# Optimization experiments

Hardware: AMD Instinct MI355X
Metric: run time of the kernel (lower is better)

Reference implementation:

```python
import jax, jax.numpy as jnp
import numpy as np

VOCAB = 28996
EMBED = 512
N = 8192


def setup_inputs() -> dict:
    key = jax.random.key(0)
    k1, k2, k3, k4 = jax.random.split(key, 4)
    x = jax.random.normal(k1, (N, EMBED), dtype=jnp.float32)
    y = jax.random.randint(k2, (N,), 0, VOCAB, dtype=jnp.int64 if jax.config.jax_enable_x64 else jnp.int32)
    # nn.Linear params: weight (vocab, embed), bias (vocab,)
    W = jax.random.normal(k3, (VOCAB, EMBED), dtype=jnp.float32) * 0.02
    b = jax.random.normal(k4, (VOCAB,), dtype=jnp.float32) * 0.02
    return {"x": x, "y": y, "W": W, "b": b}


def reference(x, y, W, b):
    # Decoder: linear -> softmax over vocab (dim=1)
    logits = jnp.einsum("ne,ve->nv", x, W) + b          # (N, VOCAB)
    probs = jax.nn.softmax(logits, axis=1)              # first softmax (faithful to original)
    # nn.CrossEntropyLoss applied to probs: mean over nodes of
    #   logsumexp(probs) - probs[y]   (i.e., -log_softmax(probs)[y])
    logp = jax.nn.log_softmax(probs, axis=1)            # second (redundant) softmax pass
    nll = -jnp.take_along_axis(logp, y[:, None].astype(jnp.int32), axis=1)[:, 0]
    return jnp.mean(nll)
```

## Files before the change

### kernel.cpp

```cpp
#include <hip/hip_runtime.h>
#include <stdint.h>

#define VOCAB 28996
#define EMBED 512
#define NROWS 8192
#define VPAD  29056
#define LOG2E 1.4426950408889634f
#define WSCALE 16.0f
#define INV_WSCALE_L2E (LOG2E / 16.0f)

typedef __attribute__((ext_vector_type(4)))  int   i32x4;
typedef __attribute__((ext_vector_type(8)))  int   i32x8;
typedef __attribute__((ext_vector_type(16))) float f32x16;

__device__ __forceinline__ void gload_lds16(const void* g, void* l) {
  __builtin_amdgcn_global_load_lds(
      (__attribute__((address_space(1))) const void*)g,
      (__attribute__((address_space(3))) void*)l, 16, 0, 0);
}

__device__ __forceinline__ int pk_fp8x4(float a, float b, float c, float d) {
  int r = __builtin_amdgcn_cvt_pk_fp8_f32(a, b, 0, false);
  r = __builtin_amdgcn_cvt_pk_fp8_f32(c, d, r, true);
  return r;
}

__global__ void __launch_bounds__(256)
prep_kernel(const float* __restrict__ x, const float* __restrict__ W,
            const float* __restrict__ b, const int* __restrict__ y,
            int* __restrict__ xb, int* __restrict__ wb,
            float* __restrict__ py, float* __restrict__ sg) {
  const int bid = blockIdx.x;
  if (bid < 7264) {
    int i = (bid * 256 + threadIdx.x) * 8;
    const int VK = VOCAB * EMBED;
    int2 o;
    if (i < VK) {
      float4 v0 = *(const float4*)(W + i);
      float4 v1 = *(const float4*)(W + i + 4);
      o.x = pk_fp8x4(v0.x * WSCALE, v0.y * WSCALE, v0.z * WSCALE, v0.w * WSCALE);
      o.y = pk_fp8x4(v1.x * WSCALE, v1.y * WSCALE, v1.z * WSCALE, v1.w * WSCALE);
    } else { o.x = 0; o.y = 0; }
    *(int2*)(wb + i / 4) = o;
  } else if (bid < 9312) {
    int i = ((bid - 7264) * 256 + threadIdx.x) * 8;
    float4 v0 = *(const float4*)(x + i);
    float4 v1 = *(const float4*)(x + i + 4);
    int2 o;
    o.x = pk_fp8x4(v0.x, v0.y, v0.z, v0.w);
    o.y = pk_fp8x4(v1.x, v1.y, v1.z, v1.w);
    *(int2*)(xb + i / 4) = o;
  } else if (bid < 11360) {
    const int row  = ((bid - 9312) * 256 + threadIdx.x) >> 6;
    const int lane = threadIdx.x & 63;
    const int yr = y[row];
    const float4* xr = (const float4*)(x + (size_t)row * EMBED);
    const float4* wr = (const float4*)(W + (size_t)yr * EMBED);
    float d = 0.f;
#pragma unroll
    for (int t = 0; t < 2; ++t) {
      float4 a = xr[lane * 2 + t], c = wr[lane * 2 + t];
      d += a.x * c.x + a.y * c.y + a.z * c.z + a.w * c.w;
    }
#pragma unroll
    for (int m = 1; m < 64; m <<= 1) d += __shfl_xor(d, m);
    if (lane == 0) py[row] = __expf(d + b[yr]);
  } else {
    int i = (bid - 11360) * 256 + threadIdx.x;
    sg[i] = 0.f;
  }
}

__global__ void __launch_bounds__(256, 4)
gemm_stats_kernel(const uint8_t* __restrict__ xb, const uint8_t* __restrict__ wb,
                  const float* __restrict__ bias, float* __restrict__ sg) {
  __shared__ uint8_t lA[128 * 128];
  __shared__ uint8_t lB[128 * 128];

  const int tid  = threadIdx.x;
  const int lane = tid & 63;
  const int w    = tid >> 6;
  const int l31  = lane & 31;
  const int h    = lane >> 5;
  const int kx   = lane & 7;
  const int wr   = (w >> 1) * 64;
  const int wc   = (w & 1) * 64;
  const int rowBase = blockIdx.x * 128;
  const int colBase = blockIdx.y * 128;

  f32x16 acc[2][2];
#pragma unroll
  for (int i = 0; i < 2; ++i)
#pragma unroll
    for (int j = 0; j < 2; ++j)
#pragma unroll
      for (int r = 0; r < 16; ++r) acc[i][j][r] = 0.f;

  const int srow = lane >> 3;
  const int skel = ((lane & 7) ^ srow) * 16;

  const int aBase = (wr + l31) * 128;
  const int bBase = (wc + l31) * 128;

  for (int kt = 0; kt < 4; ++kt) {
    const int k0 = kt * 128;
#pragma unroll
    for (int t = 0; t < 4; ++t) {
      const int c = w * 4 + t;
      const int r = c * 8 + srow;
      gload_lds16(xb + (size_t)(rowBase + r) * EMBED + k0 + skel, &lA[c * 1024]);
      gload_lds16(wb + (size_t)(colBase + r) * EMBED + k0 + skel, &lB[c * 1024]);
    }
    __syncthreads();
#pragma unroll
    for (int kk = 0; kk < 2; ++kk) {
      const int c0 = ((kk * 4 + h * 2) ^ kx) << 4;
      const int c1 = c0 ^ 16;
      i32x8 bq[2];
#pragma unroll
      for (int jj = 0; jj < 2; ++jj) {
        const int base = bBase + jj * 32 * 128;
        i32x4 lo = *(const i32x4*)&lB[base + c0];
        i32x4 hi = *(const i32x4*)&lB[base + c1];
        bq[jj] = __builtin_shufflevector(lo, hi, 0, 1, 2, 3, 4, 5, 6, 7);
      }
#pragma unroll
      for (int ii = 0; ii < 2; ++ii) {
        const int base = aBase + ii * 32 * 128;
        i32x4 lo = *(const i32x4*)&lA[base + c0];
        i32x4 hi = *(const i32x4*)&lA[base + c1];
        i32x8 af = __builtin_shufflevector(lo, hi, 0, 1, 2, 3, 4, 5, 6, 7);
        acc[ii][0] = __builtin_amdgcn_mfma_scale_f32_32x32x64_f8f6f4(
            af, bq[0], acc[ii][0], 0, 0, 0, 0x7F7F7F7F, 0, 0x7F7F7F7F);
        acc[ii][1] = __builtin_amdgcn_mfma_scale_f32_32x32x64_f8f6f4(
            af, bq[1], acc[ii][1], 0, 0, 0, 0x7F7F7F7F, 0, 0x7F7F7F7F);
      }
    }
    __syncthreads();
  }

  float bvl[2];
#pragma unroll
  for (int jj = 0; jj < 2; ++jj) {
    const int col = colBase + wc + jj * 32 + l31;
    bvl[jj] = (col < VOCAB) ? bias[col] * LOG2E : -1e30f;
  }

  float sp[32];
#pragma unroll
  for (int ii = 0; ii < 2; ++ii)
#pragma unroll
    for (int r = 0; r < 16; ++r)
      sp[ii * 16 + r] = exp2f(fmaf(acc[ii][0][r], INV_WSCALE_L2E, bvl[0])) +
                        exp2f(fmaf(acc[ii][1][r], INV_WSCALE_L2E, bvl[1]));

  float t1[16];
#pragma unroll
  for (int u = 0; u < 16; ++u) {
    float a = sp[2 * u]     + __shfl_xor(sp[2 * u],     1);
    float b = sp[2 * u + 1] + __shfl_xor(sp[2 * u + 1], 1);
    t1[u] = (l31 & 1) ? b : a;
  }
  float t2[8];
#pragma unroll
  for (int u = 0; u < 8; ++u) {
    float a = t1[2 * u]     + __shfl_xor(t1[2 * u],     2);
    float b = t1[2 * u + 1] + __shfl_xor(t1[2 * u + 1], 2);
    t2[u] = (l31 & 2) ? b : a;
  }
  float t3[4];
#pragma unroll
  for (int u = 0; u < 4; ++u) {
    float a = t2[2 * u]     + __shfl_xor(t2[2 * u],     4);
    float b = t2[2 * u + 1] + __shfl_xor(t2[2 * u + 1], 4);
    t3[u] = (l31 & 4) ? b : a;
  }
  float t4[2];
#pragma unroll
  for (int u = 0; u < 2; ++u) {
    float a = t3[2 * u]     + __shfl_xor(t3[2 * u],     8);
    float b = t3[2 * u + 1] + __shfl_xor(t3[2 * u + 1], 8);
    t4[u] = (l31 & 8) ? b : a;
  }
  {
    float a = t4[0] + __shfl_xor(t4[0], 16);
    float b = t4[1] + __shfl_xor(t4[1], 16);
    float ssum = (l31 & 16) ? b : a;
    const int v = l31;
    const int row = rowBase + wr + (v >> 4) * 32 + (v & 3) + 8 * ((v & 15) >> 2) + 4 * h;
    atomicAdd(&sg[row], ssum);
  }
}

__global__ void finalize_kernel(const float* __restrict__ sg, const float* __restrict__ py,
                                float* __restrict__ out) {
  __shared__ float red[256];
  float a = 0.f;
  for (int i = threadIdx.x; i < NROWS; i += 256)
    a += py[i] / sg[i];
  red[threadIdx.x] = a;
  __syncthreads();
  for (int st = 128; st > 0; st >>= 1) {
    if (threadIdx.x < st) red[threadIdx.x] += red[threadIdx.x + st];
    __syncthreads();
  }
  if (threadIdx.x == 0)
    out[0] = logf((float)(VOCAB + 1)) - red[0] * (1.f / (float)NROWS);
}

extern "C" void kernel_launch(void* const* d_in, const int* in_sizes, int n_in,
                              void* d_out, int out_size, void* d_ws, size_t ws_size,
                              hipStream_t stream) {
  const float* x = (const float*)d_in[0];
  const int*   y = (const int*)d_in[1];
  const float* W = (const float*)d_in[2];
  const float* b = (const float*)d_in[3];

  char* ws = (char*)d_ws;
  uint8_t* xb = (uint8_t*)ws;
  uint8_t* wb = (uint8_t*)(ws + 4194304);
  float*   sg = (float*)(ws + 4194304 + 14876672);
  float*   py = sg + NROWS;

  prep_kernel<<<11392, 256, 0, stream>>>(x, W, b, y, (int*)xb, (int*)wb, py, sg);
  gemm_stats_kernel<<<dim3(64, 227), 256, 0, stream>>>(xb, wb, b, sg);
  finalize_kernel<<<1, 256, 0, stream>>>(sg, py, (float*)d_out);
}
```

Baseline: 269.6 us.

## Fuse finalize into GEMM via last-block atomic counter; batch LDS fragment loads

Removes the separate single-block finalize launch. Each GEMM block now increments a global counter after its atomic row-sum updates, and the last block to finish computes the final loss reduction. The counter is reset in the prep kernel. Inner-loop LDS reads are also reordered so all A/B fragment halves are loaded before the MFMAs issue. The gain is one fewer kernel launch, paid for with an extra agent-scope atomic in every block.

```diff
diff --git a/kernel.cpp b/kernel.cpp
--- a/kernel.cpp
+++ b/kernel.cpp
@@ -8,6 +8,7 @@
 #define LOG2E 1.4426950408889634f
 #define WSCALE 16.0f
 #define INV_WSCALE_L2E (LOG2E / 16.0f)
+#define GEMM_BLOCKS (64 * 227)
 
 typedef __attribute__((ext_vector_type(4)))  int   i32x4;
 typedef __attribute__((ext_vector_type(8)))  int   i32x8;
@@ -29,7 +30,8 @@
 prep_kernel(const float* __restrict__ x, const float* __restrict__ W,
             const float* __restrict__ b, const int* __restrict__ y,
             int* __restrict__ xb, int* __restrict__ wb,
-            float* __restrict__ py, float* __restrict__ sg) {
+            float* __restrict__ py, float* __restrict__ sg,
+            unsigned* __restrict__ counter) {
   const int bid = blockIdx.x;
   if (bid < 7264) {
     int i = (bid * 256 + threadIdx.x) * 8;
@@ -68,14 +70,18 @@
   } else {
     int i = (bid - 11360) * 256 + threadIdx.x;
     sg[i] = 0.f;
+    if (bid == 11360 && threadIdx.x == 0) *counter = 0u;
   }
 }
 
 __global__ void __launch_bounds__(256, 4)
 gemm_stats_kernel(const uint8_t* __restrict__ xb, const uint8_t* __restrict__ wb,
-                  const float* __restrict__ bias, float* __restrict__ sg) {
+                  const float* __restrict__ bias, float* __restrict__ sg,
+                  const float* __restrict__ py, unsigned* __restrict__ counter,
+                  float* __restrict__ out) {
   __shared__ uint8_t lA[128 * 128];
   __shared__ uint8_t lB[128 * 128];
+  __shared__ bool amLast;
 
   const int tid  = threadIdx.x;
   const int lane = tid & 63;
@@ -116,24 +122,24 @@
     for (int kk = 0; kk < 2; ++kk) {
       const int c0 = ((kk * 4 + h * 2) ^ kx) << 4;
       const int c1 = c0 ^ 16;
-      i32x8 bq[2];
-#pragma unroll
-      for (int jj = 0; jj < 2; ++jj) {
-        const int base = bBase + jj * 32 * 128;
-        i32x4 lo = *(const i32x4*)&lB[base + c0];
-        i32x4 hi = *(const i32x4*)&lB[base + c1];
-        bq[jj] = __builtin_shufflevector(lo, hi, 0, 1, 2, 3, 4, 5, 6, 7);
-      }
+      i32x4 blo[2], bhi[2], alo[2], ahi[2];
+#pragma unroll
+      for (int jj = 0; jj < 2; ++jj) blo[jj] = *(const i32x4*)&lB[bBase + jj * 4096 + c0];
+#pragma unroll
+      for (int ii = 0; ii < 2; ++ii) alo[ii] = *(const i32x4*)&lA[aBase + ii * 4096 + c0];
+#pragma unroll
+      for (int jj = 0; jj < 2; ++jj) bhi[jj] = *(const i32x4*)&lB[bBase + jj * 4096 + c1];
+#pragma unroll
+      for (int ii = 0; ii < 2; ++ii) ahi[ii] = *(const i32x4*)&lA[aBase + ii * 4096 + c1];
 #pragma unroll
       for (int ii = 0; ii < 2; ++ii) {
-        const int base = aBase + ii * 32 * 128;
-        i32x4 lo = *(const i32x4*)&lA[base + c0];
-        i32x4 hi = *(const i32x4*)&lA[base + c1];
-        i32x8 af = __builtin_shufflevector(lo, hi, 0, 1, 2, 3, 4, 5, 6, 7);
-        acc[ii][0] = __builtin_amdgcn_mfma_scale_f32_32x32x64_f8f6f4(
-            af, bq[0], acc[ii][0], 0, 0, 0, 0x7F7F7F7F, 0, 0x7F7F7F7F);
-        acc[ii][1] = __builtin_amdgcn_mfma_scale_f32_32x32x64_f8f6f4(
-            af, bq[1], acc[ii][1], 0, 0, 0, 0x7F7F7F7F, 0, 0x7F7F7F7F);
+        i32x8 af = __builtin_shufflevector(alo[ii], ahi[ii], 0, 1, 2, 3, 4, 5, 6, 7);
+#pragma unroll
+        for (int jj = 0; jj < 2; ++jj) {
+          i32x8 bq = __builtin_shufflevector(blo[jj], bhi[jj], 0, 1, 2, 3, 4, 5, 6, 7);
+          acc[ii][jj] = __builtin_amdgcn_mfma_scale_f32_32x32x64_f8f6f4(
+              af, bq, acc[ii][jj], 0, 0, 0, 0x7F7F7F7F, 0, 0x7F7F7F7F);
+        }
       }
     }
     __syncthreads();
@@ -190,22 +196,29 @@
     const int row = rowBase + wr + (v >> 4) * 32 + (v & 3) + 8 * ((v & 15) >> 2) + 4 * h;
     atomicAdd(&sg[row], ssum);
   }
-}
-
-__global__ void finalize_kernel(const float* __restrict__ sg, const float* __restrict__ py,
-                                float* __restrict__ out) {
-  __shared__ float red[256];
-  float a = 0.f;
-  for (int i = threadIdx.x; i < NROWS; i += 256)
-    a += py[i] / sg[i];
-  red[threadIdx.x] = a;
+
+  if (tid == 0) {
+    unsigned old = __hip_atomic_fetch_add(counter, 1u, __ATOMIC_ACQ_REL,
+                                          __HIP_MEMORY_SCOPE_AGENT);
+    amLast = (old == (unsigned)(GEMM_BLOCKS - 1));
+  }
   __syncthreads();
-  for (int st = 128; st > 0; st >>= 1) {
-    if (threadIdx.x < st) red[threadIdx.x] += red[threadIdx.x + st];
+  if (amLast) {
+    float a = 0.f;
+    for (int i = tid; i < NROWS; i += 256) {
+      float s = __hip_atomic_load(&sg[i], __ATOMIC_RELAXED, __HIP_MEMORY_SCOPE_AGENT);
+      a += py[i] / s;
+    }
+    float* red = (float*)lA;
+    red[tid] = a;
     __syncthreads();
-  }
-  if (threadIdx.x == 0)
-    out[0] = logf((float)(VOCAB + 1)) - red[0] * (1.f / (float)NROWS);
+    for (int st = 128; st > 0; st >>= 1) {
+      if (tid < st) red[tid] += red[tid + st];
+      __syncthreads();
+    }
+    if (tid == 0)
+      out[0] = logf((float)(VOCAB + 1)) - red[0] * (1.f / (float)NROWS);
+  }
 }
 
 extern "C" void kernel_launch(void* const* d_in, const int* in_sizes, int n_in,
@@ -217,12 +230,13 @@
   const float* b = (const float*)d_in[3];
 
   char* ws = (char*)d_ws;
-  uint8_t* xb = (uint8_t*)ws;
-  uint8_t* wb = (uint8_t*)(ws + 4194304);
-  float*   sg = (float*)(ws + 4194304 + 14876672);
-  float*   py = sg + NROWS;
-
-  prep_kernel<<<11392, 256, 0, stream>>>(x, W, b, y, (int*)xb, (int*)wb, py, sg);
-  gemm_stats_kernel<<<dim3(64, 227), 256, 0, stream>>>(xb, wb, b, sg);
-  finalize_kernel<<<1, 256, 0, stream>>>(sg, py, (float*)d_out);
-}
+  uint8_t*  xb = (uint8_t*)ws;
+  uint8_t*  wb = (uint8_t*)(ws + 4194304);
+  float*    sg = (float*)(ws + 4194304 + 14876672);
+  float*    py = sg + NROWS;
+  unsigned* counter = (unsigned*)(py + NROWS);
+
+  prep_kernel<<<11392, 256, 0, stream>>>(x, W, b, y, (int*)xb, (int*)wb, py, sg, counter);
+  gemm_stats_kernel<<<dim3(64, 227), 256, 0, stream>>>(xb, wb, b, sg, py, counter,
+                                                       (float*)d_out);
+}
```

Result: slower. 470.9 us (+74.7%).

## Double-buffer LDS tiles in fp8 GEMM to overlap loads with MFMA

Applied to the files above, without the earlier changes.

Replaces the single A/B LDS tile pair with two buffer pairs and unrolls the four K-steps by hand. The global-to-LDS loads for the next K-step are issued before the MFMA work on the current step, with one barrier per step instead of two. The goal is to hide global load latency behind compute. The cost is twice the LDS per block (64 KB), which likely cuts how many blocks fit on each CU below the launch-bounds target of 4 and reduces latency hiding across blocks.

```diff
diff --git a/kernel.cpp b/kernel.cpp
--- a/kernel.cpp
+++ b/kernel.cpp
@@ -74,8 +74,7 @@
 __global__ void __launch_bounds__(256, 4)
 gemm_stats_kernel(const uint8_t* __restrict__ xb, const uint8_t* __restrict__ wb,
                   const float* __restrict__ bias, float* __restrict__ sg) {
-  __shared__ uint8_t lA[128 * 128];
-  __shared__ uint8_t lB[128 * 128];
+  __shared__ uint8_t lds[4][16384];
 
   const int tid  = threadIdx.x;
   const int lane = tid & 63;
@@ -102,16 +101,18 @@
   const int aBase = (wr + l31) * 128;
   const int bBase = (wc + l31) * 128;
 
-  for (int kt = 0; kt < 4; ++kt) {
+  auto stage = [&](int kt, uint8_t* bufA, uint8_t* bufB) {
     const int k0 = kt * 128;
 #pragma unroll
     for (int t = 0; t < 4; ++t) {
       const int c = w * 4 + t;
       const int r = c * 8 + srow;
-      gload_lds16(xb + (size_t)(rowBase + r) * EMBED + k0 + skel, &lA[c * 1024]);
-      gload_lds16(wb + (size_t)(colBase + r) * EMBED + k0 + skel, &lB[c * 1024]);
+      gload_lds16(xb + (size_t)(rowBase + r) * EMBED + k0 + skel, &bufA[c * 1024]);
+      gload_lds16(wb + (size_t)(colBase + r) * EMBED + k0 + skel, &bufB[c * 1024]);
     }
-    __syncthreads();
+  };
+
+  auto compute = [&](const uint8_t* bufA, const uint8_t* bufB) {
 #pragma unroll
     for (int kk = 0; kk < 2; ++kk) {
       const int c0 = ((kk * 4 + h * 2) ^ kx) << 4;
@@ -119,16 +120,16 @@
       i32x8 bq[2];
 #pragma unroll
       for (int jj = 0; jj < 2; ++jj) {
-        const int base = bBase + jj * 32 * 128;
-        i32x4 lo = *(const i32x4*)&lB[base + c0];
-        i32x4 hi = *(const i32x4*)&lB[base + c1];
+        const int base = bBase + jj * 4096;
+        i32x4 lo = *(const i32x4*)&bufB[base + c0];
+        i32x4 hi = *(const i32x4*)&bufB[base + c1];
         bq[jj] = __builtin_shufflevector(lo, hi, 0, 1, 2, 3, 4, 5, 6, 7);
       }
 #pragma unroll
       for (int ii = 0; ii < 2; ++ii) {
-        const int base = aBase + ii * 32 * 128;
-        i32x4 lo = *(const i32x4*)&lA[base + c0];
-        i32x4 hi = *(const i32x4*)&lA[base + c1];
+        const int base = aBase + ii * 4096;
+        i32x4 lo = *(const i32x4*)&bufA[base + c0];
+        i32x4 hi = *(const i32x4*)&bufA[base + c1];
         i32x8 af = __builtin_shufflevector(lo, hi, 0, 1, 2, 3, 4, 5, 6, 7);
         acc[ii][0] = __builtin_amdgcn_mfma_scale_f32_32x32x64_f8f6f4(
             af, bq[0], acc[ii][0], 0, 0, 0, 0x7F7F7F7F, 0, 0x7F7F7F7F);
@@ -136,8 +137,20 @@
             af, bq[1], acc[ii][1], 0, 0, 0, 0x7F7F7F7F, 0, 0x7F7F7F7F);
       }
     }
-    __syncthreads();
-  }
+  };
+
+  stage(0, lds[0], lds[1]);
+  __syncthreads();
+  stage(1, lds[2], lds[3]);
+  compute(lds[0], lds[1]);
+  __syncthreads();
+  stage(2, lds[0], lds[1]);
+  compute(lds[2], lds[3]);
+  __syncthreads();
+  stage(3, lds[2], lds[3]);
+  compute(lds[0], lds[1]);
+  __syncthreads();
+  compute(lds[2], lds[3]);
 
   float bvl[2];
 #pragma unroll
```

Measured after the change: 311.5 us. 1.16x slower.

## Pre-tile FP8 operands in MFMA fragment order and load directly to registers

Applied to the files above, without the earlier changes.

The prep kernel now writes the FP8 copies of x and W in a tiled layout that matches the per-lane fragment order of the 32x32x64 MFMA. The GEMM then reads each fragment straight from global memory into registers, with no LDS staging and no barriers, and unrolls all 8 K-steps. This removes the shared-memory round trip and the __syncthreads stalls. In exchange, operands are no longer shared through LDS, so every wave fetches its own data from global memory or cache, and the launch-bounds occupancy hint drops from 4 to 3.

```diff
diff --git a/kernel.cpp b/kernel.cpp
--- a/kernel.cpp
+++ b/kernel.cpp
@@ -13,22 +13,21 @@
 typedef __attribute__((ext_vector_type(8)))  int   i32x8;
 typedef __attribute__((ext_vector_type(16))) float f32x16;
 
-__device__ __forceinline__ void gload_lds16(const void* g, void* l) {
-  __builtin_amdgcn_global_load_lds(
-      (__attribute__((address_space(1))) const void*)g,
-      (__attribute__((address_space(3))) void*)l, 16, 0, 0);
-}
-
 __device__ __forceinline__ int pk_fp8x4(float a, float b, float c, float d) {
   int r = __builtin_amdgcn_cvt_pk_fp8_f32(a, b, 0, false);
   r = __builtin_amdgcn_cvt_pk_fp8_f32(c, d, r, true);
   return r;
 }
 
+__device__ __forceinline__ size_t tile_dst(int r, int o) {
+  return (size_t)((r >> 5) * 8 + (o >> 6)) * 2048 +
+         (((o >> 5) & 1) * 32 + (r & 31)) * 32 + (o & 31);
+}
+
 __global__ void __launch_bounds__(256)
 prep_kernel(const float* __restrict__ x, const float* __restrict__ W,
             const float* __restrict__ b, const int* __restrict__ y,
-            int* __restrict__ xb, int* __restrict__ wb,
+            uint8_t* __restrict__ xT, uint8_t* __restrict__ wT,
             float* __restrict__ py, float* __restrict__ sg) {
   const int bid = blockIdx.x;
   if (bid < 7264) {
@@ -41,7 +40,7 @@
       o.x = pk_fp8x4(v0.x * WSCALE, v0.y * WSCALE, v0.z * WSCALE, v0.w * WSCALE);
       o.y = pk_fp8x4(v1.x * WSCALE, v1.y * WSCALE, v1.z * WSCALE, v1.w * WSCALE);
     } else { o.x = 0; o.y = 0; }
-    *(int2*)(wb + i / 4) = o;
+    *(int2*)(wT + tile_dst(i >> 9, i & 511)) = o;
   } else if (bid < 9312) {
     int i = ((bid - 7264) * 256 + threadIdx.x) * 8;
     float4 v0 = *(const float4*)(x + i);
@@ -49,7 +48,7 @@
     int2 o;
     o.x = pk_fp8x4(v0.x, v0.y, v0.z, v0.w);
     o.y = pk_fp8x4(v1.x, v1.y, v1.z, v1.w);
-    *(int2*)(xb + i / 4) = o;
+    *(int2*)(xT + tile_dst(i >> 9, i & 511)) = o;
   } else if (bid < 11360) {
     const int row  = ((bid - 9312) * 256 + threadIdx.x) >> 6;
     const int lane = threadIdx.x & 63;
@@ -71,23 +70,22 @@
   }
 }
 
-__global__ void __launch_bounds__(256, 4)
-gemm_stats_kernel(const uint8_t* __restrict__ xb, const uint8_t* __restrict__ wb,
+__global__ void __launch_bounds__(256, 3)
+gemm_stats_kernel(const uint8_t* __restrict__ xT, const uint8_t* __restrict__ wT,
                   const float* __restrict__ bias, float* __restrict__ sg) {
-  __shared__ uint8_t lA[128 * 128];
-  __shared__ uint8_t lB[128 * 128];
-
   const int tid  = threadIdx.x;
   const int lane = tid & 63;
   const int w    = tid >> 6;
   const int l31  = lane & 31;
   const int h    = lane >> 5;
-  const int kx   = lane & 7;
   const int wr   = (w >> 1) * 64;
   const int wc   = (w & 1) * 64;
   const int rowBase = blockIdx.x * 128;
   const int colBase = blockIdx.y * 128;
 
+  const uint8_t* aT = xT + ((size_t)(((rowBase + wr) >> 5) * 8)) * 2048 + lane * 32;
+  const uint8_t* bT = wT + ((size_t)(((colBase + wc) >> 5) * 8)) * 2048 + lane * 32;
+
   f32x16 acc[2][2];
 #pragma unroll
   for (int i = 0; i < 2; ++i)
@@ -96,47 +94,28 @@
 #pragma unroll
       for (int r = 0; r < 16; ++r) acc[i][j][r] = 0.f;
 
-  const int srow = lane >> 3;
-  const int skel = ((lane & 7) ^ srow) * 16;
-
-  const int aBase = (wr + l31) * 128;
-  const int bBase = (wc + l31) * 128;
-
-  for (int kt = 0; kt < 4; ++kt) {
-    const int k0 = kt * 128;
-#pragma unroll
-    for (int t = 0; t < 4; ++t) {
-      const int c = w * 4 + t;
-      const int r = c * 8 + srow;
-      gload_lds16(xb + (size_t)(rowBase + r) * EMBED + k0 + skel, &lA[c * 1024]);
-      gload_lds16(wb + (size_t)(colBase + r) * EMBED + k0 + skel, &lB[c * 1024]);
+#pragma unroll
+  for (int s = 0; s < 8; ++s) {
+    const int offs = s * 2048;
+    i32x8 af[2], bq[2];
+#pragma unroll
+    for (int ii = 0; ii < 2; ++ii) {
+      i32x4 lo = *(const i32x4*)(aT + ii * 16384 + offs);
+      i32x4 hi = *(const i32x4*)(aT + ii * 16384 + offs + 16);
+      af[ii] = __builtin_shufflevector(lo, hi, 0, 1, 2, 3, 4, 5, 6, 7);
     }
-    __syncthreads();
-#pragma unroll
-    for (int kk = 0; kk < 2; ++kk) {
-      const int c0 = ((kk * 4 + h * 2) ^ kx) << 4;
-      const int c1 = c0 ^ 16;
-      i32x8 bq[2];
-#pragma unroll
-      for (int jj = 0; jj < 2; ++jj) {
-        const int base = bBase + jj * 32 * 128;
-        i32x4 lo = *(const i32x4*)&lB[base + c0];
-        i32x4 hi = *(const i32x4*)&lB[base + c1];
-        bq[jj] = __builtin_shufflevector(lo, hi, 0, 1, 2, 3, 4, 5, 6, 7);
-      }
-#pragma unroll
-      for (int ii = 0; ii < 2; ++ii) {
-        const int base = aBase + ii * 32 * 128;
-        i32x4 lo = *(const i32x4*)&lA[base + c0];
-        i32x4 hi = *(const i32x4*)&lA[base + c1];
-        i32x8 af = __builtin_shufflevector(lo, hi, 0, 1, 2, 3, 4, 5, 6, 7);
-        acc[ii][0] = __builtin_amdgcn_mfma_scale_f32_32x32x64_f8f6f4(
-            af, bq[0], acc[ii][0], 0, 0, 0, 0x7F7F7F7F, 0, 0x7F7F7F7F);
-        acc[ii][1] = __builtin_amdgcn_mfma_scale_f32_32x32x64_f8f6f4(
-            af, bq[1], acc[ii][1], 0, 0, 0, 0x7F7F7F7F, 0, 0x7F7F7F7F);
-      }
+#pragma unroll
+    for (int jj = 0; jj < 2; ++jj) {
+      i32x4 lo = *(const i32x4*)(bT + jj * 16384 + offs);
+      i32x4 hi = *(const i32x4*)(bT + jj * 16384 + offs + 16);
+      bq[jj] = __builtin_shufflevector(lo, hi, 0, 1, 2, 3, 4, 5, 6, 7);
     }
-    __syncthreads();
+#pragma unroll
+    for (int ii = 0; ii < 2; ++ii)
+#pragma unroll
+      for (int jj = 0; jj < 2; ++jj)
+        acc[ii][jj] = __builtin_amdgcn_mfma_scale_f32_32x32x64_f8f6f4(
+            af[ii], bq[jj], acc[ii][jj], 0, 0, 0, 0x7F7F7F7F, 0, 0x7F7F7F7F);
   }
 
   float bvl[2];
@@ -217,12 +196,12 @@
   const float* b = (const float*)d_in[3];
 
   char* ws = (char*)d_ws;
-  uint8_t* xb = (uint8_t*)ws;
-  uint8_t* wb = (uint8_t*)(ws + 4194304);
+  uint8_t* xT = (uint8_t*)ws;
+  uint8_t* wT = (uint8_t*)(ws + 4194304);
   float*   sg = (float*)(ws + 4194304 + 14876672);
   float*   py = sg + NROWS;
 
-  prep_kernel<<<11392, 256, 0, stream>>>(x, W, b, y, (int*)xb, (int*)wb, py, sg);
-  gemm_stats_kernel<<<dim3(64, 227), 256, 0, stream>>>(xb, wb, b, sg);
+  prep_kernel<<<11392, 256, 0, stream>>>(x, W, b, y, xT, wT, py, sg);
+  gemm_stats_kernel<<<dim3(64, 227), 256, 0, stream>>>(xT, wT, b, sg);
   finalize_kernel<<<1, 256, 0, stream>>>(sg, py, (float*)d_out);
 }
```

After: 281.7 us. 1.04x slower.
